# Kernel optimization log

Hardware: AMD Instinct MI355X
Metric: run time of the kernel (lower is better)

Reference implementation:

```python
import jax, jax.numpy as jnp
import numpy as np

VOCAB, EMB, HID, K = 50000, 300, 512, 12
START, STOP = 10, 11
B, T = 64, 256
NEG = -10000.0


def _lstm_scan(x_tbe, h0, c0, w_ih, w_hh, b):
    """One-direction LSTM. x_tbe: [T,B,E]; returns hidden states [T,B,H].
    PyTorch gate order: i, f, g, o."""
    def step(carry, xt):
        h, c = carry
        z = xt @ w_ih.T + h @ w_hh.T + b  # [B,4H]
        i, f, g, o = jnp.split(z, 4, axis=-1)
        c = jax.nn.sigmoid(f) * c + jax.nn.sigmoid(i) * jnp.tanh(g)
        h = jax.nn.sigmoid(o) * jnp.tanh(c)
        return (h, c), h
    _, hs = jax.lax.scan(step, (h0, c0), x_tbe)
    return hs


def _viterbi(feats, transitions):
    """Batched Viterbi decode. feats: [B,T,K]. Returns (score[B], paths[B,T])."""
    b = feats.shape[0]
    init = jnp.full((b, K), NEG, feats.dtype).at[:, START].set(0.0)

    def step(fv, feat_t):
        # scores[b, next, prev] = fv[b, prev] + transitions[next, prev]
        scores = fv[:, None, :] + transitions[None, :, :]
        bp = jnp.argmax(scores, axis=2)                  # [B,K] backpointers
        fv = jnp.max(scores, axis=2) + feat_t            # [B,K]
        return fv, bp

    fv, bps = jax.lax.scan(step, init, feats.transpose(1, 0, 2))  # bps: [T,B,K]
    term = fv + transitions[STOP][None, :]
    best = jnp.argmax(term, axis=1)                      # [B]
    score = jnp.max(term, axis=1)                        # [B]

    def back(tag, bp):
        prev = jnp.take_along_axis(bp, tag[:, None], axis=1)[:, 0]
        return prev, tag

    _, ys = jax.lax.scan(back, best, bps[::-1])          # ys: [T,B], last->first
    paths = ys[::-1].transpose(1, 0)                     # [B,T]
    return score, paths


def setup_inputs() -> dict:
    key = jax.random.key(0)
    ks = jax.random.split(key, 16)
    H = HID // 2
    s = 0.1
    rn = lambda k, shp, sc=s: jax.random.normal(k, shp, dtype=jnp.float32) * sc
    trans = jax.random.normal(ks[2], (K, K), dtype=jnp.float32)
    trans = trans.at[START, :].set(NEG).at[:, STOP].set(NEG)
    return {
        "sentence": jax.random.randint(ks[0], (B, T), 0, VOCAB),
        "embed": rn(ks[1], (VOCAB, EMB), 1.0),
        "w_ih_f": rn(ks[3], (4 * H, EMB)), "w_hh_f": rn(ks[4], (4 * H, H)),
        "b_ih_f": rn(ks[5], (4 * H,)), "b_hh_f": rn(ks[6], (4 * H,)),
        "w_ih_b": rn(ks[7], (4 * H, EMB)), "w_hh_b": rn(ks[8], (4 * H, H)),
        "b_ih_b": rn(ks[9], (4 * H,)), "b_hh_b": rn(ks[10], (4 * H,)),
        "w_out": rn(ks[11], (K, HID)), "b_out": rn(ks[12], (K,)),
        "transitions": trans,
        "h0": rn(ks[13], (2, B, H), 1.0),
        "c0": rn(ks[14], (2, B, H), 1.0),
    }


def reference(sentence, embed, w_ih_f, w_hh_f, b_ih_f, b_hh_f,
              w_ih_b, w_hh_b, b_ih_b, b_hh_b, w_out, b_out,
              transitions, h0, c0):
    x = embed[sentence].transpose(1, 0, 2)               # [T,B,E]
    hf = _lstm_scan(x, h0[0], c0[0], w_ih_f, w_hh_f, b_ih_f + b_hh_f)
    hb = _lstm_scan(x[::-1], h0[1], c0[1], w_ih_b, w_hh_b, b_ih_b + b_hh_b)[::-1]
    out = jnp.concatenate([hf, hb], axis=-1).transpose(1, 0, 2)  # [B,T,HID]
    feats = out @ w_out.T + b_out                        # [B,T,K]
    score, paths = _viterbi(feats, transitions)
    return score, paths
```

## Files before the change

kernel.cpp:

```cpp
#include <hip/hip_runtime.h>

#define BB   64
#define TT   256
#define EE   300
#define EP   320
#define HH   256
#define ZN   1024
#define KK   12
#define TAG_START 10
#define TAG_STOP  11
#define NEGV -10000.0f

#define OFF_XPAD  0ull
#define OFF_WIH   10485760ull
#define OFF_ZX    11796480ull
#define OFF_HF    78905344ull
#define OFF_HB    87326720ull
#define OFF_BIAS  95748096ull
#define OFF_WOUT  95756288ull
#define OFF_FEATS 95772672ull
#define WS_NEED   96561152ull

typedef __attribute__((ext_vector_type(8))) short short8;
typedef __attribute__((ext_vector_type(4))) float f32x4;
typedef __attribute__((ext_vector_type(2))) float f32x2;
typedef __attribute__((ext_vector_type(4))) unsigned short u16x4;
typedef __attribute__((ext_vector_type(2))) unsigned short u16x2;

__device__ __forceinline__ unsigned short f2bf(float f) {
    unsigned x; __builtin_memcpy(&x, &f, 4);
    x += 0x7fffu + ((x >> 16) & 1u);
    return (unsigned short)(x >> 16);
}
__device__ __forceinline__ float bf2f(unsigned short u) {
    unsigned x = ((unsigned)u) << 16;
    float f; __builtin_memcpy(&f, &x, 4);
    return f;
}
__device__ __forceinline__ float rcpf_(float x) { return __builtin_amdgcn_rcpf(x); }
__device__ __forceinline__ float sigmoidf_(float x) {
    return rcpf_(1.0f + __expf(-x));
}
__device__ __forceinline__ float tanhf_(float x) {
    float e = __expf(-2.0f * fabsf(x));
    float r = (1.0f - e) * rcpf_(1.0f + e);
    return copysignf(r, x);
}

__global__ __launch_bounds__(256) void gather_kernel(
    const int* __restrict__ sent, const float* __restrict__ embed,
    unsigned short* __restrict__ xpad)
{
    int r = blockIdx.x;
    int t = r >> 6, b = r & 63;
    int tok = sent[b * TT + t];
    const float* src = embed + (size_t)tok * EE;
    unsigned short* dst = xpad + (size_t)r * EP;
    for (int c = threadIdx.x; c < EP; c += 256)
        dst[c] = (c < EE) ? f2bf(src[c]) : (unsigned short)0;
}

__global__ __launch_bounds__(256) void prep_kernel(
    const float* __restrict__ wih_f, const float* __restrict__ wih_b,
    const float* __restrict__ bih_f, const float* __restrict__ bhh_f,
    const float* __restrict__ bih_b, const float* __restrict__ bhh_b,
    const float* __restrict__ wout,
    const float* __restrict__ whh_f, const float* __restrict__ whh_b,
    unsigned short* __restrict__ wih_pad, float* __restrict__ bias,
    unsigned short* __restrict__ wout_pad, unsigned short* __restrict__ whh_str)
{
    int i = blockIdx.x * 256 + threadIdx.x;
    if (i < 2048 * EP) {
        int rr = i / EP, c = i - rr * EP;
        int dir = rr >> 10, r = rr & 1023;
        const float* w = dir ? wih_b : wih_f;
        wih_pad[i] = (c < EE) ? f2bf(w[r * EE + c]) : (unsigned short)0;
        return;
    }
    i -= 2048 * EP;
    if (i < 2 * ZN) {
        int dir = i >> 10, z = i & 1023;
        bias[i] = dir ? (bih_b[z] + bhh_b[z]) : (bih_f[z] + bhh_f[z]);
        return;
    }
    i -= 2 * ZN;
    if (i < 16 * 512) {
        int r = i >> 9, c = i & 511;
        wout_pad[i] = (r < KK) ? f2bf(wout[r * 512 + c]) : (unsigned short)0;
        return;
    }
    i -= 16 * 512;
    if (i < 2 * 1024 * 64) {
        int dir = i >> 16, rem = i & 65535;
        int zr = rem >> 6, kc = rem & 63;
        const float* w = dir ? whh_b : whh_f;
        whh_str[i] = f2bf(w[(size_t)zr * 256 + 192 + kc]);
    }
}

__global__ __launch_bounds__(256) void gemm_zx(
    const unsigned short* __restrict__ xpad,
    const unsigned short* __restrict__ wih_pad,
    const float* __restrict__ bias,
    unsigned short* __restrict__ zx)
{
    int bid = blockIdx.x;
    int tm = bid & 255, tn = bid >> 8;
    int lane = threadIdx.x & 63, w = threadIdx.x >> 6;
    int lm = lane & 15, lk = lane >> 4;
    int n0 = tn * 64 + w * 16;

    f32x4 acc[4];
#pragma unroll
    for (int m = 0; m < 4; m++) acc[m] = (f32x4){0.f, 0.f, 0.f, 0.f};

#pragma unroll
    for (int kk = 0; kk < 10; kk++) {
        short8 bf = *(const short8*)(wih_pad + (size_t)(n0 + lm) * EP + kk * 32 + lk * 8);
#pragma unroll
        for (int m = 0; m < 4; m++) {
            short8 af = *(const short8*)(xpad + (size_t)(tm * 64 + m * 16 + lm) * EP + kk * 32 + lk * 8);
            acc[m] = __builtin_amdgcn_mfma_f32_16x16x32_bf16(af, bf, acc[m], 0, 0, 0);
        }
    }
    int zc = n0 + lm;
    int dirz = zc >> 10, rem = zc & 1023, g = rem >> 8, hc = rem & 255;
    float bv = bias[zc];
#pragma unroll
    for (int m = 0; m < 4; m++)
#pragma unroll
        for (int r = 0; r < 4; r++) {
            int row = tm * 64 + m * 16 + lk * 4 + r;
            zx[(size_t)row * 2048 + dirz * 1024 + hc * 4 + g] = f2bf(acc[m][r] + bv);
        }
}

__global__ __launch_bounds__(512)
__attribute__((amdgpu_waves_per_eu(2, 2)))
void lstm_rec(
    const unsigned short* __restrict__ zx,
    const float* __restrict__ whh_f, const float* __restrict__ whh_b,
    const unsigned short* __restrict__ whh_str,
    const float* __restrict__ h0, const float* __restrict__ c0,
    unsigned short* __restrict__ hf_hist, unsigned short* __restrict__ hb_hist)
{
    const int bid = blockIdx.x;
    const int dir = bid & 1, bg = bid >> 1;
    const int tid = threadIdx.x;
    const int w = tid >> 6, lane = tid & 63;
    const int lm = lane & 15, lk = lane >> 4;

    __shared__ __align__(16) unsigned char wlds[128 * 1024];
    __shared__ __align__(16) unsigned char hbuf[8192];
    __shared__ __align__(16) float zlds[4 * 4 * 256];

    const float* whh = dir ? whh_b : whh_f;
    unsigned short* hist = dir ? hb_hist : hf_hist;
    const unsigned short* wstr = whh_str + dir * 65536;

    short8 wreg[32];
#pragma unroll
    for (int tau = 0; tau < 8; tau++) {
        const int zr = (tau >> 1) * 256 + w * 32 + (tau & 1) * 16 + lm;
#pragma unroll
        for (int kt = 0; kt < 6; kt++) {
            const float* s = whh + (size_t)zr * 256 + kt * 32 + lk * 8;
            f32x4 lo = *(const f32x4*)s;
            f32x4 hi = *(const f32x4*)(s + 4);
            short8 f;
#pragma unroll
            for (int e = 0; e < 4; e++) { f[e] = (short)f2bf(lo[e]); f[4 + e] = (short)f2bf(hi[e]); }
            if (kt < 4) wreg[tau * 4 + kt] = f;
            else *(short8*)(wlds + (size_t)(((w * 2 + (kt - 4)) * 8 + tau) * 64 + lane) * 16) = f;
        }
    }

    const int gb = tid & 3;
    const int hc0 = (tid >> 2) * 2;
    const int B = bg * 4 + gb;
    const int hoff = (hc0 >> 5) * 1024 + ((hc0 >> 3) & 3) * 256 + gb * 16 + (hc0 & 7) * 2;

    *(uint4*)(hbuf + tid * 16) = (uint4){0u, 0u, 0u, 0u};
    __syncthreads();
    f32x2 cv = *(const f32x2*)(c0 + ((size_t)dir * BB + B) * HH + hc0);
    f32x2 hv0 = *(const f32x2*)(h0 + ((size_t)dir * BB + B) * HH + hc0);
    float c0r = cv[0], c1r = cv[1];
    *(u16x2*)(hbuf + hoff) = (u16x2){f2bf(hv0[0]), f2bf(hv0[1])};
    __syncthreads();

#pragma unroll 1
    for (int s = 0; s < TT; s++) {
        const int t = dir ? (TT - 1 - s) : s;
        const int wslot = dir ? t : (s + 1);

        short8 zxv = *(const short8*)(zx + ((size_t)t * BB + B) * 2048 + dir * ZN + hc0 * 4);

#pragma unroll
        for (int pass = 0; pass < 2; pass++) {
            short8 wg6[4], wg7[4];
#pragma unroll
            for (int g = 0; g < 4; g++) {
                const int zr = g * 256 + w * 32 + pass * 16 + lm;
                wg6[g] = *(const short8*)(wstr + (size_t)zr * 64 + lk * 8);
                wg7[g] = *(const short8*)(wstr + (size_t)zr * 64 + 32 + lk * 8);
            }

            f32x4 acc[4];
#pragma unroll
            for (int g = 0; g < 4; g++) acc[g] = (f32x4){0.f, 0.f, 0.f, 0.f};

#pragma unroll
            for (int kt = 0; kt < 8; kt++) {
                short8 hb = *(const short8*)(hbuf + kt * 1024 + lane * 16);
#pragma unroll
                for (int g = 0; g < 4; g++) {
                    const int tau = g * 2 + pass;
                    short8 a;
                    if (kt < 4)       a = wreg[tau * 4 + kt];
                    else if (kt < 6)  a = *(const short8*)(wlds + (size_t)(((w * 2 + (kt - 4)) * 8 + tau) * 64 + lane) * 16);
                    else if (kt == 6) a = wg6[g];
                    else              a = wg7[g];
                    acc[g] = __builtin_amdgcn_mfma_f32_16x16x32_bf16(a, hb, acc[g], 0, 0, 0);
                }
            }

            if (lm < 4) {
                const int hcb = w * 32 + pass * 16 + lk * 4;
#pragma unroll
                for (int g = 0; g < 4; g++)
                    *(f32x4*)&zlds[(g * 4 + lm) * 256 + (hcb ^ (lm * 8))] = acc[g];
            }
        }
        __syncthreads();

        f32x2 zrr[4];
#pragma unroll
        for (int g = 0; g < 4; g++)
            zrr[g] = *(const f32x2*)&zlds[(g * 4 + gb) * 256 + (hc0 ^ (gb * 8))];

        u16x2 hv;
        {
            float zi = zrr[0][0] + bf2f((unsigned short)zxv[0]);
            float zf = zrr[1][0] + bf2f((unsigned short)zxv[1]);
            float zg = zrr[2][0] + bf2f((unsigned short)zxv[2]);
            float zo = zrr[3][0] + bf2f((unsigned short)zxv[3]);
            float cc = sigmoidf_(zf) * c0r + sigmoidf_(zi) * tanhf_(zg);
            c0r = cc;
            hv[0] = f2bf(sigmoidf_(zo) * tanhf_(cc));
        }
        {
            float zi = zrr[0][1] + bf2f((unsigned short)zxv[4]);
            float zf = zrr[1][1] + bf2f((unsigned short)zxv[5]);
            float zg = zrr[2][1] + bf2f((unsigned short)zxv[6]);
            float zo = zrr[3][1] + bf2f((unsigned short)zxv[7]);
            float cc = sigmoidf_(zf) * c1r + sigmoidf_(zi) * tanhf_(zg);
            c1r = cc;
            hv[1] = f2bf(sigmoidf_(zo) * tanhf_(cc));
        }
        *(u16x2*)(hbuf + hoff) = hv;
        *(u16x2*)(hist + ((size_t)wslot * BB + B) * HH + hc0) = hv;

        __syncthreads();
    }
}

__global__ __launch_bounds__(256) void feats_kernel(
    const unsigned short* __restrict__ hf_hist, const unsigned short* __restrict__ hb_hist,
    const unsigned short* __restrict__ wout_pad, const float* __restrict__ b_out,
    float* __restrict__ feats)
{
    const int tid = threadIdx.x, lane = tid & 63, w = tid >> 6;
    const int lm = lane & 15, lk = lane >> 4;
    const int r0 = blockIdx.x * 64;

    __shared__ float red[4][64][16];

    const unsigned short* hsrc = (w < 2) ? (hf_hist + BB * HH) : hb_hist;
    const int kb = (w & 1) * 128;

    f32x4 acc[4];
#pragma unroll
    for (int m = 0; m < 4; m++) acc[m] = (f32x4){0.f, 0.f, 0.f, 0.f};

#pragma unroll
    for (int kk = 0; kk < 4; kk++) {
        short8 bf = *(const short8*)(wout_pad + (size_t)lm * 512 + w * 128 + kk * 32 + lk * 8);
#pragma unroll
        for (int m = 0; m < 4; m++) {
            short8 a = *(const short8*)(hsrc + (size_t)(r0 + m * 16 + lm) * HH + kb + kk * 32 + lk * 8);
            acc[m] = __builtin_amdgcn_mfma_f32_16x16x32_bf16(a, bf, acc[m], 0, 0, 0);
        }
    }
#pragma unroll
    for (int m = 0; m < 4; m++)
#pragma unroll
        for (int r = 0; r < 4; r++)
            red[w][m * 16 + lk * 4 + r][lm] = acc[m][r];
    __syncthreads();

#pragma unroll
    for (int q = 0; q < 4; q++) {
        int e = tid + q * 256;
        int row = e >> 4, col = e & 15;
        if (col < KK) {
            float v = red[0][row][col] + red[1][row][col] + red[2][row][col] + red[3][row][col]
                      + b_out[col];
            int gr = r0 + row, t = gr >> 6, bb = gr & 63;
            feats[(size_t)bb * TT * KK + t * KK + col] = v;
        }
    }
}

__global__ __launch_bounds__(256) void viterbi_kernel(
    const float* __restrict__ feats, const float* __restrict__ trans,
    float* __restrict__ out)
{
    __shared__ float fl[4][TT * KK];
    __shared__ unsigned char bp[4][TT][KK];
    const int tid = threadIdx.x, lane = tid & 63, v = tid >> 6;
    const int b = blockIdx.x * 4 + v;

    for (int i = lane; i < TT * KK; i += 64) fl[v][i] = feats[(size_t)b * TT * KK + i];
    __syncthreads();

    float trow[12] = {0};
    float tstop = 0.f;
    if (lane < KK) {
#pragma unroll
        for (int p = 0; p < KK; p++) trow[p] = trans[lane * KK + p];
        tstop = trans[TAG_STOP * KK + lane];
    }
    float fv = (lane == TAG_START) ? 0.0f : NEGV;

    for (int t = 0; t < TT; t++) {
        float best = -3.0e38f; int arg = 0;
#pragma unroll
        for (int p = 0; p < KK; p++) {
            float sc = __shfl(fv, p, 64) + trow[p];
            if (sc > best) { best = sc; arg = p; }
        }
        if (lane < KK) {
            bp[v][t][lane] = (unsigned char)arg;
            fv = best + fl[v][t * KK + lane];
        }
    }

    float term = fv + tstop;
    float best = -3.0e38f; int arg = 0;
#pragma unroll
    for (int p = 0; p < KK; p++) {
        float sc = __shfl(term, p, 64);
        if (sc > best) { best = sc; arg = p; }
    }
    if (lane == 0) {
        out[b] = best;
        int tag = arg;
        for (int t = TT - 1; t >= 0; t--) {
            out[BB + (size_t)b * TT + t] = (float)tag;
            if (t > 0) tag = bp[v][t][tag];
        }
    }
}

extern "C" void kernel_launch(void* const* d_in, const int* in_sizes, int n_in,
                              void* d_out, int out_size, void* d_ws, size_t ws_size,
                              hipStream_t stream)
{
    (void)in_sizes; (void)n_in; (void)out_size;
    const int*   sent  = (const int*)d_in[0];
    const float* embed = (const float*)d_in[1];
    const float* wih_f = (const float*)d_in[2];
    const float* whh_f = (const float*)d_in[3];
    const float* bih_f = (const float*)d_in[4];
    const float* bhh_f = (const float*)d_in[5];
    const float* wih_b = (const float*)d_in[6];
    const float* whh_b = (const float*)d_in[7];
    const float* bih_b = (const float*)d_in[8];
    const float* bhh_b = (const float*)d_in[9];
    const float* wout  = (const float*)d_in[10];
    const float* bout  = (const float*)d_in[11];
    const float* trans = (const float*)d_in[12];
    const float* h0    = (const float*)d_in[13];
    const float* c0    = (const float*)d_in[14];
    float* out = (float*)d_out;

    if (ws_size < WS_NEED) return;

    char* ws = (char*)d_ws;
    unsigned short* xpad     = (unsigned short*)(ws + OFF_XPAD);
    unsigned short* wih_pad  = (unsigned short*)(ws + OFF_WIH);
    unsigned short* zx       = (unsigned short*)(ws + OFF_ZX);
    unsigned short* hf_hist  = (unsigned short*)(ws + OFF_HF);
    unsigned short* hb_hist  = (unsigned short*)(ws + OFF_HB);
    float*          bias     = (float*)(ws + OFF_BIAS);
    unsigned short* wout_pad = (unsigned short*)(ws + OFF_WOUT);
    float*          feats    = (float*)(ws + OFF_FEATS);
    unsigned short* whh_str  = (unsigned short*)(ws + OFF_FEATS);

    gather_kernel<<<TT * BB, 256, 0, stream>>>(sent, embed, xpad);
    prep_kernel<<<(2048 * EP + 2 * ZN + 16 * 512 + 2 * 1024 * 64 + 255) / 256, 256, 0, stream>>>(
        wih_f, wih_b, bih_f, bhh_f, bih_b, bhh_b, wout, whh_f, whh_b,
        wih_pad, bias, wout_pad, whh_str);
    gemm_zx<<<256 * 32, 256, 0, stream>>>(xpad, wih_pad, bias, zx);
    lstm_rec<<<32, 512, 0, stream>>>(zx, whh_f, whh_b, whh_str, h0, c0, hf_hist, hb_hist);
    feats_kernel<<<256, 256, 0, stream>>>(hf_hist, hb_hist, wout_pad, bout, feats);
    viterbi_kernel<<<16, 256, 0, stream>>>(feats, trans, out);
}
```

Measured before the change: 830.3 us.

## Rebalance LSTM recurrent weights across registers, LDS and global; merge gate passes

Changes how the recurrent weight matrix is stored in the LSTM recurrence kernel. Five k-tiles now live in registers (was four) and two in LDS, so only the last k-tile is streamed from global memory each step. The two gate passes are merged into one loop with eight accumulators, and pointer arithmetic is strength-reduced. The __syncthreads calls become explicit lgkmcnt-wait barriers that avoid waiting on global stores. The trade-off is much higher register pressure (40 weight vectors plus 8 accumulators), which risks spills.

```diff
diff --git a/kernel.cpp b/kernel.cpp
--- a/kernel.cpp
+++ b/kernel.cpp
@@ -47,6 +47,13 @@
     return copysignf(r, x);
 }
 
+__device__ __forceinline__ void lds_barrier() {
+    __builtin_amdgcn_sched_barrier(0);
+    asm volatile("s_waitcnt lgkmcnt(0)" ::: "memory");
+    __builtin_amdgcn_s_barrier();
+    __builtin_amdgcn_sched_barrier(0);
+}
+
 __global__ __launch_bounds__(256) void gather_kernel(
     const int* __restrict__ sent, const float* __restrict__ embed,
     unsigned short* __restrict__ xpad)
@@ -90,11 +97,11 @@
         return;
     }
     i -= 16 * 512;
-    if (i < 2 * 1024 * 64) {
-        int dir = i >> 16, rem = i & 65535;
-        int zr = rem >> 6, kc = rem & 63;
+    if (i < 2 * 1024 * 32) {
+        int dir = i >> 15, rem = i & 32767;
+        int zr = rem >> 5, kc = rem & 31;
         const float* w = dir ? whh_b : whh_f;
-        whh_str[i] = f2bf(w[(size_t)zr * 256 + 192 + kc]);
+        whh_str[i] = f2bf(w[(size_t)zr * 256 + 224 + kc]);
     }
 }
 
@@ -150,28 +157,28 @@
     const int w = tid >> 6, lane = tid & 63;
     const int lm = lane & 15, lk = lane >> 4;
 
-    __shared__ __align__(16) unsigned char wlds[128 * 1024];
+    __shared__ __align__(16) unsigned char wlds[131072];
     __shared__ __align__(16) unsigned char hbuf[8192];
     __shared__ __align__(16) float zlds[4 * 4 * 256];
 
     const float* whh = dir ? whh_b : whh_f;
     unsigned short* hist = dir ? hb_hist : hf_hist;
-    const unsigned short* wstr = whh_str + dir * 65536;
-
-    short8 wreg[32];
+    const unsigned short* wstr = whh_str + dir * 32768;
+
+    short8 wreg[40];
 #pragma unroll
     for (int tau = 0; tau < 8; tau++) {
         const int zr = (tau >> 1) * 256 + w * 32 + (tau & 1) * 16 + lm;
 #pragma unroll
-        for (int kt = 0; kt < 6; kt++) {
+        for (int kt = 0; kt < 7; kt++) {
             const float* s = whh + (size_t)zr * 256 + kt * 32 + lk * 8;
             f32x4 lo = *(const f32x4*)s;
             f32x4 hi = *(const f32x4*)(s + 4);
             short8 f;
 #pragma unroll
             for (int e = 0; e < 4; e++) { f[e] = (short)f2bf(lo[e]); f[4 + e] = (short)f2bf(hi[e]); }
-            if (kt < 4) wreg[tau * 4 + kt] = f;
-            else *(short8*)(wlds + (size_t)(((w * 2 + (kt - 4)) * 8 + tau) * 64 + lane) * 16) = f;
+            if (kt < 5) wreg[tau * 5 + kt] = f;
+            else *(short8*)(wlds + (size_t)(((w * 2 + (kt - 5)) * 8 + tau) * 64 + lane) * 16) = f;
         }
     }
 
@@ -188,50 +195,52 @@
     *(u16x2*)(hbuf + hoff) = (u16x2){f2bf(hv0[0]), f2bf(hv0[1])};
     __syncthreads();
 
+    const int t0 = dir ? (TT - 1) : 0;
+    const int ws0 = dir ? (TT - 1) : 1;
+    const long zd = (long)(dir ? -1 : 1) * BB * 2048;
+    const long hd = (long)(dir ? -1 : 1) * BB * HH;
+    const unsigned short* zp = zx + ((size_t)t0 * BB + B) * 2048 + dir * ZN + hc0 * 4;
+    unsigned short* hw = hist + ((size_t)ws0 * BB + B) * HH + hc0;
+
 #pragma unroll 1
     for (int s = 0; s < TT; s++) {
-        const int t = dir ? (TT - 1 - s) : s;
-        const int wslot = dir ? t : (s + 1);
-
-        short8 zxv = *(const short8*)(zx + ((size_t)t * BB + B) * 2048 + dir * ZN + hc0 * 4);
-
-#pragma unroll
-        for (int pass = 0; pass < 2; pass++) {
-            short8 wg6[4], wg7[4];
-#pragma unroll
-            for (int g = 0; g < 4; g++) {
-                const int zr = g * 256 + w * 32 + pass * 16 + lm;
-                wg6[g] = *(const short8*)(wstr + (size_t)zr * 64 + lk * 8);
-                wg7[g] = *(const short8*)(wstr + (size_t)zr * 64 + 32 + lk * 8);
+        short8 zxv = *(const short8*)zp;
+
+        const unsigned short* wsp = wstr;
+        asm volatile("" : "+v"(wsp));
+        short8 wg[8];
+#pragma unroll
+        for (int tau = 0; tau < 8; tau++) {
+            const int zr = (tau >> 1) * 256 + w * 32 + (tau & 1) * 16 + lm;
+            wg[tau] = *(const short8*)(wsp + (size_t)zr * 32 + lk * 8);
+        }
+
+        f32x4 acc[8];
+#pragma unroll
+        for (int tau = 0; tau < 8; tau++) acc[tau] = (f32x4){0.f, 0.f, 0.f, 0.f};
+
+#pragma unroll
+        for (int kt = 0; kt < 8; kt++) {
+            short8 hb = *(const short8*)(hbuf + kt * 1024 + lane * 16);
+#pragma unroll
+            for (int tau = 0; tau < 8; tau++) {
+                short8 a;
+                if (kt < 5)       a = wreg[tau * 5 + kt];
+                else if (kt < 7)  a = *(const short8*)(wlds + (size_t)(((w * 2 + (kt - 5)) * 8 + tau) * 64 + lane) * 16);
+                else              a = wg[tau];
+                acc[tau] = __builtin_amdgcn_mfma_f32_16x16x32_bf16(a, hb, acc[tau], 0, 0, 0);
             }
-
-            f32x4 acc[4];
-#pragma unroll
-            for (int g = 0; g < 4; g++) acc[g] = (f32x4){0.f, 0.f, 0.f, 0.f};
-
-#pragma unroll
-            for (int kt = 0; kt < 8; kt++) {
-                short8 hb = *(const short8*)(hbuf + kt * 1024 + lane * 16);
-#pragma unroll
-                for (int g = 0; g < 4; g++) {
-                    const int tau = g * 2 + pass;
-                    short8 a;
-                    if (kt < 4)       a = wreg[tau * 4 + kt];
-                    else if (kt < 6)  a = *(const short8*)(wlds + (size_t)(((w * 2 + (kt - 4)) * 8 + tau) * 64 + lane) * 16);
-                    else if (kt == 6) a = wg6[g];
-                    else              a = wg7[g];
-                    acc[g] = __builtin_amdgcn_mfma_f32_16x16x32_bf16(a, hb, acc[g], 0, 0, 0);
-                }
+        }
+
+        if (lm < 4) {
+#pragma unroll
+            for (int tau = 0; tau < 8; tau++) {
+                const int g = tau >> 1;
+                const int hcb = w * 32 + (tau & 1) * 16 + lk * 4;
+                *(f32x4*)&zlds[(g * 4 + lm) * 256 + (hcb ^ (lm * 8))] = acc[tau];
             }
-
-            if (lm < 4) {
-                const int hcb = w * 32 + pass * 16 + lk * 4;
-#pragma unroll
-                for (int g = 0; g < 4; g++)
-                    *(f32x4*)&zlds[(g * 4 + lm) * 256 + (hcb ^ (lm * 8))] = acc[g];
-            }
-        }
-        __syncthreads();
+        }
+        lds_barrier();
 
         f32x2 zrr[4];
 #pragma unroll
@@ -258,9 +267,12 @@
             hv[1] = f2bf(sigmoidf_(zo) * tanhf_(cc));
         }
         *(u16x2*)(hbuf + hoff) = hv;
-        *(u16x2*)(hist + ((size_t)wslot * BB + B) * HH + hc0) = hv;
-
-        __syncthreads();
+        *(u16x2*)hw = hv;
+
+        lds_barrier();
+
+        zp += zd;
+        hw += hd;
     }
 }
 
@@ -398,7 +410,7 @@
     unsigned short* whh_str  = (unsigned short*)(ws + OFF_FEATS);
 
     gather_kernel<<<TT * BB, 256, 0, stream>>>(sent, embed, xpad);
-    prep_kernel<<<(2048 * EP + 2 * ZN + 16 * 512 + 2 * 1024 * 64 + 255) / 256, 256, 0, stream>>>(
+    prep_kernel<<<(2048 * EP + 2 * ZN + 16 * 512 + 2 * 1024 * 32 + 255) / 256, 256, 0, stream>>>(
         wih_f, wih_b, bih_f, bhh_f, bih_b, bhh_b, wout, whh_f, whh_b,
         wih_pad, bias, wout_pad, whh_str);
     gemm_zx<<<256 * 32, 256, 0, stream>>>(xpad, wih_pad, bias, zx);
```

Result: slower. 916.6 us (+10.4%).

## Double-buffer LSTM hidden state and keep gate exchange wave-local to drop a barrier

Applied to the files above, without the earlier changes.

Restructures the recurrent LSTM step so each wave computes the gate nonlinearities for its own hidden columns straight from its MFMA outputs through a per-wave LDS scratch. This removes the block-wide barrier between the matmul and the elementwise phase. The hidden state is double-buffered in LDS, so each timestep needs one barrier (a custom lgkmcnt wait plus s_barrier) instead of two. It also preloads all eight h fragments up front and uses strength-reduced pointers for zx and the history writes. The risks are higher register pressure and correctness depending on the wave-local zlds indexing matching the new lane-to-column mapping.

```diff
diff --git a/kernel.cpp b/kernel.cpp
--- a/kernel.cpp
+++ b/kernel.cpp
@@ -47,6 +47,13 @@
     return copysignf(r, x);
 }
 
+__device__ __forceinline__ void lds_barrier() {
+    __builtin_amdgcn_sched_barrier(0);
+    asm volatile("s_waitcnt lgkmcnt(0)" ::: "memory");
+    __builtin_amdgcn_s_barrier();
+    __builtin_amdgcn_sched_barrier(0);
+}
+
 __global__ __launch_bounds__(256) void gather_kernel(
     const int* __restrict__ sent, const float* __restrict__ embed,
     unsigned short* __restrict__ xpad)
@@ -150,9 +157,9 @@
     const int w = tid >> 6, lane = tid & 63;
     const int lm = lane & 15, lk = lane >> 4;
 
-    __shared__ __align__(16) unsigned char wlds[128 * 1024];
-    __shared__ __align__(16) unsigned char hbuf[8192];
-    __shared__ __align__(16) float zlds[4 * 4 * 256];
+    __shared__ __align__(16) unsigned char wlds[131072];
+    __shared__ __align__(16) unsigned char hbuf[2][8192];
+    __shared__ __align__(16) float zlds[2048];
 
     const float* whh = dir ? whh_b : whh_f;
     unsigned short* hist = dir ? hb_hist : hf_hist;
@@ -175,25 +182,49 @@
         }
     }
 
-    const int gb = tid & 3;
-    const int hc0 = (tid >> 2) * 2;
+    const int gb = lane & 3;
+    const int hcl = lane >> 2;
     const int B = bg * 4 + gb;
-    const int hoff = (hc0 >> 5) * 1024 + ((hc0 >> 3) & 3) * 256 + gb * 16 + (hc0 & 7) * 2;
-
-    *(uint4*)(hbuf + tid * 16) = (uint4){0u, 0u, 0u, 0u};
+    const int hoff0 = w * 1024 + (hcl >> 3) * 256 + gb * 16 + (hcl & 7) * 2;
+    const int hoff1 = hoff0 + 512;
+    float* zw = zlds + w * 256;
+
+    *(uint4*)(hbuf[0] + tid * 16) = (uint4){0u, 0u, 0u, 0u};
+    *(uint4*)(hbuf[1] + tid * 16) = (uint4){0u, 0u, 0u, 0u};
     __syncthreads();
-    f32x2 cv = *(const f32x2*)(c0 + ((size_t)dir * BB + B) * HH + hc0);
-    f32x2 hv0 = *(const f32x2*)(h0 + ((size_t)dir * BB + B) * HH + hc0);
-    float c0r = cv[0], c1r = cv[1];
-    *(u16x2*)(hbuf + hoff) = (u16x2){f2bf(hv0[0]), f2bf(hv0[1])};
+    float c0r, c1r;
+    {
+        const float* hp = h0 + ((size_t)dir * BB + B) * HH + w * 32 + hcl;
+        const float* cp = c0 + ((size_t)dir * BB + B) * HH + w * 32 + hcl;
+        c0r = cp[0]; c1r = cp[16];
+        *(unsigned short*)(hbuf[0] + hoff0) = f2bf(hp[0]);
+        *(unsigned short*)(hbuf[0] + hoff1) = f2bf(hp[16]);
+    }
     __syncthreads();
+
+    const int t0 = dir ? (TT - 1) : 0;
+    const int ws0 = dir ? (TT - 1) : 1;
+    const long zd = (long)(dir ? -1 : 1) * BB * 2048;
+    const long hd = (long)(dir ? -1 : 1) * BB * HH;
+    const unsigned short* zp = zx + ((size_t)t0 * BB + B) * 2048 + dir * 1024 + (w * 32 + hcl) * 4;
+    unsigned short* hw = hist + ((size_t)ws0 * BB + B) * HH + w * 32 + hcl;
+    int cur = 0;
 
 #pragma unroll 1
     for (int s = 0; s < TT; s++) {
-        const int t = dir ? (TT - 1 - s) : s;
-        const int wslot = dir ? t : (s + 1);
-
-        short8 zxv = *(const short8*)(zx + ((size_t)t * BB + B) * 2048 + dir * ZN + hc0 * 4);
+        u16x4 zxv0 = *(const u16x4*)zp;
+        u16x4 zxv1 = *(const u16x4*)(zp + 64);
+
+        const unsigned char* rb = hbuf[cur];
+        unsigned char* wb = hbuf[cur ^ 1];
+
+        short8 hb[8];
+#pragma unroll
+        for (int kt = 0; kt < 8; kt++)
+            hb[kt] = *(const short8*)(rb + kt * 1024 + lane * 16);
+
+        const unsigned short* wsp = wstr;
+        asm volatile("" : "+v"(wsp));
 
 #pragma unroll
         for (int pass = 0; pass < 2; pass++) {
@@ -201,8 +232,8 @@
 #pragma unroll
             for (int g = 0; g < 4; g++) {
                 const int zr = g * 256 + w * 32 + pass * 16 + lm;
-                wg6[g] = *(const short8*)(wstr + (size_t)zr * 64 + lk * 8);
-                wg7[g] = *(const short8*)(wstr + (size_t)zr * 64 + 32 + lk * 8);
+                wg6[g] = *(const short8*)(wsp + (size_t)zr * 64 + lk * 8);
+                wg7[g] = *(const short8*)(wsp + (size_t)zr * 64 + 32 + lk * 8);
             }
 
             f32x4 acc[4];
@@ -211,7 +242,6 @@
 
 #pragma unroll
             for (int kt = 0; kt < 8; kt++) {
-                short8 hb = *(const short8*)(hbuf + kt * 1024 + lane * 16);
 #pragma unroll
                 for (int g = 0; g < 4; g++) {
                     const int tau = g * 2 + pass;
@@ -220,47 +250,38 @@
                     else if (kt < 6)  a = *(const short8*)(wlds + (size_t)(((w * 2 + (kt - 4)) * 8 + tau) * 64 + lane) * 16);
                     else if (kt == 6) a = wg6[g];
                     else              a = wg7[g];
-                    acc[g] = __builtin_amdgcn_mfma_f32_16x16x32_bf16(a, hb, acc[g], 0, 0, 0);
+                    acc[g] = __builtin_amdgcn_mfma_f32_16x16x32_bf16(a, hb[kt], acc[g], 0, 0, 0);
                 }
             }
 
             if (lm < 4) {
-                const int hcb = w * 32 + pass * 16 + lk * 4;
 #pragma unroll
                 for (int g = 0; g < 4; g++)
-                    *(f32x4*)&zlds[(g * 4 + lm) * 256 + (hcb ^ (lm * 8))] = acc[g];
+                    *(f32x4*)&zw[g * 64 + lm * 16 + ((lk * 4) ^ (lm * 4))] = acc[g];
             }
-        }
-        __syncthreads();
-
-        f32x2 zrr[4];
-#pragma unroll
-        for (int g = 0; g < 4; g++)
-            zrr[g] = *(const f32x2*)&zlds[(g * 4 + gb) * 256 + (hc0 ^ (gb * 8))];
-
-        u16x2 hv;
-        {
-            float zi = zrr[0][0] + bf2f((unsigned short)zxv[0]);
-            float zf = zrr[1][0] + bf2f((unsigned short)zxv[1]);
-            float zg = zrr[2][0] + bf2f((unsigned short)zxv[2]);
-            float zo = zrr[3][0] + bf2f((unsigned short)zxv[3]);
-            float cc = sigmoidf_(zf) * c0r + sigmoidf_(zi) * tanhf_(zg);
-            c0r = cc;
-            hv[0] = f2bf(sigmoidf_(zo) * tanhf_(cc));
-        }
-        {
-            float zi = zrr[0][1] + bf2f((unsigned short)zxv[4]);
-            float zf = zrr[1][1] + bf2f((unsigned short)zxv[5]);
-            float zg = zrr[2][1] + bf2f((unsigned short)zxv[6]);
-            float zo = zrr[3][1] + bf2f((unsigned short)zxv[7]);
-            float cc = sigmoidf_(zf) * c1r + sigmoidf_(zi) * tanhf_(zg);
-            c1r = cc;
-            hv[1] = f2bf(sigmoidf_(zo) * tanhf_(cc));
-        }
-        *(u16x2*)(hbuf + hoff) = hv;
-        *(u16x2*)(hist + ((size_t)wslot * BB + B) * HH + hc0) = hv;
-
-        __syncthreads();
+
+            float z0 = zw[0 * 64 + gb * 16 + (hcl ^ (gb * 4))];
+            float z1 = zw[1 * 64 + gb * 16 + (hcl ^ (gb * 4))];
+            float z2 = zw[2 * 64 + gb * 16 + (hcl ^ (gb * 4))];
+            float z3 = zw[3 * 64 + gb * 16 + (hcl ^ (gb * 4))];
+
+            u16x4 zxv = pass ? zxv1 : zxv0;
+            float cin = pass ? c1r : c0r;
+            float zi = z0 + bf2f(zxv[0]);
+            float zf = z1 + bf2f(zxv[1]);
+            float zg = z2 + bf2f(zxv[2]);
+            float zo = z3 + bf2f(zxv[3]);
+            float cc = sigmoidf_(zf) * cin + sigmoidf_(zi) * tanhf_(zg);
+            if (pass) c1r = cc; else c0r = cc;
+            unsigned short hv = f2bf(sigmoidf_(zo) * tanhf_(cc));
+            *(unsigned short*)(wb + (pass ? hoff1 : hoff0)) = hv;
+            hw[pass * 16] = hv;
+        }
+
+        lds_barrier();
+        cur ^= 1;
+        zp += zd;
+        hw += hd;
     }
 }
 
```

Result: slower. 1.504 ms (+81.2%).
